# Performance work log

Measured on AMD Instinct MI355X. Metric: run time of the kernel, lower is better.

The kernel has to match this reference:

```python
import jax, jax.numpy as jnp
import numpy as np

TRIM_RATIO = 0.1
B, N, D_IN, D_H, N_OUT, D_OUT = 64, 1024, 512, 1024, 10, 1


def setup_inputs() -> dict:
    key = jax.random.key(0)
    ks = jax.random.split(key, 10)
    X = jax.random.normal(ks[0], (B, N, D_IN), dtype=jnp.float32)
    # ragged valid lengths in [N//2, N]; guarantees num_valid > 2*k for trim_ratio=0.1
    lengths = jax.random.randint(ks[1], (B,), N // 2, N + 1)
    mask = (jnp.arange(N)[None, :] < lengths[:, None]).astype(jnp.float32)
    s_in, s_h = 1.0 / np.sqrt(D_IN), 1.0 / np.sqrt(D_H)
    W1 = jax.random.uniform(ks[2], (D_IN, D_H), jnp.float32, -s_in, s_in)
    b1 = jax.random.uniform(ks[3], (D_H,), jnp.float32, -s_in, s_in)
    W2 = jax.random.uniform(ks[4], (D_H, D_H), jnp.float32, -s_h, s_h)
    b2 = jax.random.uniform(ks[5], (D_H,), jnp.float32, -s_h, s_h)
    W3 = jax.random.uniform(ks[6], (D_H, D_H), jnp.float32, -s_h, s_h)
    b3 = jax.random.uniform(ks[7], (D_H,), jnp.float32, -s_h, s_h)
    W4 = jax.random.uniform(ks[8], (D_H, N_OUT * D_OUT), jnp.float32, -s_h, s_h)
    b4 = jax.random.uniform(ks[9], (N_OUT * D_OUT,), jnp.float32, -s_h, s_h)
    return {"X": X, "mask": mask, "W1": W1, "b1": b1, "W2": W2, "b2": b2,
            "W3": W3, "b3": b3, "W4": W4, "b4": b4}


def reference(X, mask, W1, b1, W2, b2, W3, b3, W4, b4):
    # encode MLP: [B,N,D_IN] -> [B,N,D_H]
    encoded = jax.nn.relu(jnp.einsum('bni,ih->bnh', X, W1) + b1) @ W2 + b2
    masked = encoded * mask[..., None]
    num_valid = mask.sum(axis=-1).astype(jnp.int32)                 # [B]
    k = (num_valid.astype(jnp.float32) * TRIM_RATIO).astype(jnp.int32)  # floor, as int()
    # push invalid rows to +inf so valid elements occupy the first num_valid slots after sort
    padded = jnp.where(mask[..., None] > 0, masked, jnp.inf)
    sorted_v = jnp.sort(padded, axis=1)                             # per-column sort, [B,N,D_H]
    pos = jnp.arange(N)[None, :]
    keep = (pos >= k[:, None]) & (pos < (num_valid - k)[:, None])   # [B,N]
    summed = jnp.sum(jnp.where(keep[..., None], sorted_v, 0.0), axis=1)  # [B,D_H]
    denom = (num_valid - 2 * k).astype(jnp.float32)[:, None]
    aggregated = summed / denom                                     # trimmed mean
    # decode MLP
    out = jax.nn.relu(aggregated @ W3 + b3) @ W4 + b4               # [B, N_OUT*D_OUT]
    out = out.reshape(-1, N_OUT, D_OUT).squeeze(-1)                 # [B, N_OUT]
    return out
```

## Files before the change

kernel.cpp:

```cpp
#include <hip/hip_runtime.h>


typedef _Float16 half8  __attribute__((ext_vector_type(8)));
typedef _Float16 half4v __attribute__((ext_vector_type(4)));
typedef float    floatx4 __attribute__((ext_vector_type(4)));

#define GLD_LDS(g, l)                                                                     \
  __builtin_amdgcn_global_load_lds((const __attribute__((address_space(1))) void*)(g),    \
                                   (__attribute__((address_space(3))) void*)(l), 16, 0, 0)

__global__ void prep_nv(const float* __restrict__ mask, int* __restrict__ nv_arr,
                        int* __restrict__ k_arr) {
  int b = blockIdx.x, lane = threadIdx.x;
  const float4* mp = (const float4*)(mask + (b << 10));
  float s = 0.f;
#pragma unroll
  for (int i = 0; i < 4; ++i) {
    float4 v = mp[lane + i * 64];
    s += v.x + v.y + v.z + v.w;
  }
#pragma unroll
  for (int off = 32; off > 0; off >>= 1) s += __shfl_xor(s, off, 64);
  if (lane == 0) {
    int nv = (int)(s + 0.5f);
    int kk = (int)((float)nv * 0.1f);
    nv_arr[b] = nv;
    k_arr[b] = kk;
  }
}

__device__ __forceinline__ void transpose_body(const float* __restrict__ W,
                                               _Float16* __restrict__ WT, int R, int C,
                                               int r0, int c0, _Float16 (*tile)[65]) {
  for (int i = threadIdx.x; i < 4096; i += 256) {
    int r = i >> 6, c = i & 63;
    tile[r][c] = (_Float16)W[(size_t)(r0 + r) * C + c0 + c];
  }
  __syncthreads();
  for (int i = threadIdx.x; i < 4096; i += 256) {
    int c = i >> 6, r = i & 63;
    WT[(size_t)(c0 + c) * R + r0 + r] = tile[r][c];
  }
}

__global__ __launch_bounds__(256) void preprocess(
    const float* __restrict__ X, _Float16* __restrict__ X16,
    const float* __restrict__ W1, _Float16* __restrict__ W1T,
    const float* __restrict__ W2, _Float16* __restrict__ W2T,
    const int* __restrict__ nv_arr) {
  __shared__ _Float16 tile[64][65];
  int bid = blockIdx.x;
  if (bid < 16384) {
    int n0 = (bid << 2) & 1023;
    int batch = bid >> 8;
    int nv = nv_arr[batch];
    if (n0 >= ((nv + 255) & ~255)) return;
    int i = (bid * 256 + threadIdx.x) * 8;
    float4 a = *(const float4*)(X + i);
    float4 c = *(const float4*)(X + i + 4);
    half8 h;
    h[0] = (_Float16)a.x; h[1] = (_Float16)a.y; h[2] = (_Float16)a.z; h[3] = (_Float16)a.w;
    h[4] = (_Float16)c.x; h[5] = (_Float16)c.y; h[6] = (_Float16)c.z; h[7] = (_Float16)c.w;
    *(half8*)(X16 + i) = h;
  } else if (bid < 16384 + 128) {
    int id = bid - 16384;
    transpose_body(W1, W1T, 512, 1024, (id & 7) * 64, (id >> 3) * 64, tile);
  } else {
    int id = bid - 16512;
    transpose_body(W2, W2T, 1024, 1024, (id & 15) * 64, (id >> 4) * 64, tile);
  }
}

template <int KDIM, int MODE>
__global__ __launch_bounds__(512, 2) void gemm_kernel(
    const _Float16* __restrict__ Aop, const _Float16* __restrict__ Bop,
    const float* __restrict__ bias, const int* __restrict__ nv_arr,
    _Float16* __restrict__ outp) {
  constexpr int NT = KDIM / 64;
  __shared__ __align__(16) _Float16 lds[2][2][256 * 64];

  int bid = blockIdx.x;
  int fat = ((((bid >> 5) << 3) | (bid & 7))) << 8;
  int thin = ((bid >> 3) & 3) << 8;
  int i0, j0;
  if (MODE == 1) {
    i0 = thin; j0 = fat;
    if ((j0 & 1023) >= nv_arr[j0 >> 10]) return;
  } else {
    i0 = fat; j0 = thin;
    if ((i0 & 1023) >= nv_arr[i0 >> 10]) return;
  }
  const int t = threadIdx.x, lane = t & 63;
  const int wv = t >> 6, wm = wv & 1, wn = wv >> 1;
  const int lr = lane & 15, q = lane >> 4;
  const int swz = (q ^ (lr & 7)) * 8;

  const int gch = (t & 7) ^ ((t >> 3) & 7);
  const _Float16* gA = Aop + (size_t)(i0 + (t >> 3)) * KDIM + gch * 8;
  const _Float16* gB = Bop + (size_t)(j0 + (t >> 3)) * KDIM + gch * 8;

#define STG(OP, BUF, KT, R)                                                   \
  GLD_LDS(((OP) ? gB : gA) + (size_t)(R) * 64 * KDIM + (size_t)(KT) * 64,     \
          &lds[BUF][OP][((R) * 512 + (t & ~63)) * 8])

  floatx4 acc[8][4] = {};
  half8 af[4][2];
  half8 bf[2][2][2];

#define LD_A(BUF, IH)                                                         \
  _Pragma("unroll") for (int f = 0; f < 4; ++f)                               \
  _Pragma("unroll") for (int kk = 0; kk < 2; ++kk)                            \
      af[f][kk] = *(const half8*)&lds[BUF][0]                                 \
          [(((wm << 7) + ((IH) << 6) + (f << 4) + lr) << 6) + (swz ^ (kk << 5))];

#define LD_B(BUF, JH)                                                         \
  _Pragma("unroll") for (int g = 0; g < 2; ++g)                               \
  _Pragma("unroll") for (int kk = 0; kk < 2; ++kk)                            \
      bf[JH][g][kk] = *(const half8*)&lds[BUF][1]                             \
          [(((wn << 6) + ((JH) << 5) + (g << 4) + lr) << 6) + (swz ^ (kk << 5))];

#define MFMA_QUAD(IH, JH)                                                     \
  _Pragma("unroll") for (int f = 0; f < 4; ++f)                               \
  _Pragma("unroll") for (int g = 0; g < 2; ++g)                               \
  _Pragma("unroll") for (int kk = 0; kk < 2; ++kk)                            \
      acc[((IH) << 2) + f][((JH) << 1) + g] =                                 \
          __builtin_amdgcn_mfma_f32_16x16x32_f16(                             \
              af[f][kk], bf[JH][g][kk], acc[((IH) << 2) + f][((JH) << 1) + g], 0, 0, 0);

#define PHASE_TAIL(IH, JH)                                                    \
  __builtin_amdgcn_s_barrier();                                               \
  asm volatile("s_waitcnt lgkmcnt(0)" ::: "memory");                          \
  __builtin_amdgcn_sched_barrier(0);                                          \
  __builtin_amdgcn_s_setprio(1);                                              \
  MFMA_QUAD(IH, JH);                                                          \
  __builtin_amdgcn_s_setprio(0);                                              \
  __builtin_amdgcn_s_barrier();

#define BODY(KT, CUR, NXT, DO_A, DO_B, VMC)                                   \
  {                                                                           \
    LD_A(CUR, 0); LD_B(CUR, 0);                                               \
    if (DO_A) { STG(0, NXT, (KT) + 1, 0); STG(0, NXT, (KT) + 1, 1); }         \
    PHASE_TAIL(0, 0);                                                         \
    LD_B(CUR, 1);                                                             \
    if (DO_A) { STG(0, NXT, (KT) + 1, 2); STG(0, NXT, (KT) + 1, 3); }         \
    PHASE_TAIL(0, 1);                                                         \
    LD_A(CUR, 1);                                                             \
    if (DO_B) { STG(1, CUR, (KT) + 2, 0); STG(1, CUR, (KT) + 2, 1); }         \
    PHASE_TAIL(1, 0);                                                         \
    if (DO_B) { STG(1, CUR, (KT) + 2, 2); STG(1, CUR, (KT) + 2, 3); }         \
    asm volatile("s_waitcnt " VMC ::: "memory");                              \
    __builtin_amdgcn_sched_barrier(0);                                        \
    __builtin_amdgcn_s_setprio(1);                                            \
    MFMA_QUAD(1, 1);                                                          \
    __builtin_amdgcn_s_setprio(0);                                            \
    __builtin_amdgcn_s_barrier();                                             \
  }

  STG(0, 0, 0, 0); STG(0, 0, 0, 1); STG(0, 0, 0, 2); STG(0, 0, 0, 3);
  STG(1, 0, 0, 0); STG(1, 0, 0, 1); STG(1, 0, 0, 2); STG(1, 0, 0, 3);
  STG(1, 1, 1, 0); STG(1, 1, 1, 1); STG(1, 1, 1, 2); STG(1, 1, 1, 3);
  asm volatile("s_waitcnt vmcnt(4)" ::: "memory");
  __builtin_amdgcn_s_barrier();

  for (int kt = 0; kt < NT - 3; kt += 2) {
    BODY(kt, 0, 1, 1, 1, "vmcnt(4)");
    BODY(kt + 1, 1, 0, 1, 1, "vmcnt(4)");
  }
  BODY(NT - 2, 0, 1, 1, 0, "vmcnt(0)");
  BODY(NT - 1, 1, 0, 0, 0, "vmcnt(0)");

  if (MODE == 1) {
#pragma unroll
    for (int mi = 0; mi < 8; ++mi) {
      int ih = i0 + (wm << 7) + (mi << 4) + (q << 2);
      floatx4 bb = *(const floatx4*)&bias[ih];
#pragma unroll
      for (int nj = 0; nj < 4; ++nj) {
        int j = j0 + (wn << 6) + (nj << 4) + lr;
        floatx4 v = acc[mi][nj];
        half4v hv;
#pragma unroll
        for (int r = 0; r < 4; ++r) hv[r] = (_Float16)fmaxf(v[r] + bb[r], 0.f);
        *(half4v*)&outp[(size_t)j * 1024 + ih] = hv;
      }
    }
  } else {
#pragma unroll
    for (int nj = 0; nj < 4; ++nj) {
      int j = j0 + (wn << 6) + (nj << 4) + lr;
      float bj = bias[j];
#pragma unroll
      for (int mi = 0; mi < 8; ++mi) {
        int im = i0 + (wm << 7) + (mi << 4) + (q << 2);
        int bb = im >> 10, n = im & 1023;
        floatx4 v = acc[mi][nj];
        half4v hv;
#pragma unroll
        for (int r = 0; r < 4; ++r) hv[r] = (_Float16)(v[r] + bj);
        *(half4v*)&outp[((size_t)bb << 20) + ((size_t)j << 10) + (size_t)n] = hv;
      }
    }
  }
}

#define NB 1024
__global__ __launch_bounds__(256) void trim_kernel(const _Float16* __restrict__ encT,
                                                   const int* __restrict__ nv_arr,
                                                   const int* __restrict__ k_arr,
                                                   float* __restrict__ agg) {
  __shared__ unsigned int cnt[4 * NB];
  int t = threadIdx.x, lane = t & 63, w = t >> 6;
  int blk = blockIdx.x;
  int batch = blk >> 8;
  int h = ((blk & 255) << 2) + w;
  unsigned int* cw = cnt + w * NB;
  uint4* cp = (uint4*)cw;
  {
    uint4 z = {0u, 0u, 0u, 0u};
#pragma unroll
    for (int i = 0; i < 4; ++i) cp[lane * 4 + (i ^ ((lane >> 1) & 3))] = z;
  }

  int nv = nv_arr[batch], kk = k_arr[batch];
  const _Float16* col = encT + ((size_t)batch << 20) + ((size_t)h << 10);
  const uint4* p = (const uint4*)col + lane * 2;
  uint4 u0 = p[0], u1 = p[1];
  unsigned vals[8] = {u0.x, u0.y, u0.z, u0.w, u1.x, u1.y, u1.z, u1.w};
  int nvalid = nv - lane * 16;

  float vv[16];
  int bn[16];
#pragma unroll
  for (int d = 0; d < 8; ++d) {
    unsigned u = vals[d];
#pragma unroll
    for (int sub = 0; sub < 2; ++sub) {
      int idx = d * 2 + sub;
      unsigned short bits = (unsigned short)(sub ? (u >> 16) : (u & 0xffffu));
      _Float16 hvv;
      __builtin_memcpy(&hvv, &bits, 2);
      float v = (float)hvv;
      if (idx < nvalid) {
        v = fminf(fmaxf(v, -8.0f), 7.999f);
        int bin = (int)((v + 8.0f) * 64.0f);
        bin = min(NB - 1, bin);
        vv[idx] = v;
        bn[idx] = bin;
        int Lb = bin >> 4, jc = (bin >> 2) & 3;
        int phys = ((Lb << 2) + (jc ^ ((Lb >> 1) & 3))) * 4 + (bin & 3);
        atomicAdd(&cw[phys], 1u);
      } else {
        vv[idx] = 0.f;
        bn[idx] = -1;
      }
    }
  }

  int c[16];
  {
    uint4 rb[4];
#pragma unroll
    for (int i = 0; i < 4; ++i) rb[i] = cp[lane * 4 + (i ^ ((lane >> 1) & 3))];
#pragma unroll
    for (int i = 0; i < 4; ++i) {
      c[4 * i] = (int)rb[i].x; c[4 * i + 1] = (int)rb[i].y;
      c[4 * i + 2] = (int)rb[i].z; c[4 * i + 3] = (int)rb[i].w;
    }
  }
  int ct = 0;
#pragma unroll
  for (int i = 0; i < 16; ++i) ct += c[i];
  int ci = ct;
#pragma unroll
  for (int off = 1; off < 64; off <<= 1) {
    int cu = __shfl_up(ci, off, 64);
    if (lane >= off) ci += cu;
  }
  int cex = ci - ct;
  int r1 = kk, r2 = nv - kk;
  int p1 = -1, p2 = -1;
  {
    int run = cex;
#pragma unroll
    for (int i = 0; i < 16; ++i) {
      int cc = c[i];
      if (run < r1 && r1 <= run + cc) p1 = ((lane * 16 + i) << 12) | run;
      if (run < r2 && r2 <= run + cc) p2 = ((lane * 16 + i) << 12) | run;
      run += cc;
    }
  }
#pragma unroll
  for (int off = 32; off > 0; off >>= 1) {
    p1 = max(p1, __shfl_xor(p1, off, 64));
    p2 = max(p2, __shfl_xor(p2, off, 64));
  }
  int b1 = p1 >> 12, cex1 = p1 & 4095;
  int b2 = p2 >> 12, cex2 = p2 & 4095;
  float s1 = 0.f, s2 = 0.f, tm = 0.f;
  int c1 = 0, c2 = 0;
#pragma unroll
  for (int i = 0; i < 16; ++i) {
    int b = bn[i];
    float v = vv[i];
    if (b == b1) { s1 += v; c1++; }
    if (b == b2) { s2 += v; c2++; }
    if (b > b1 && b < b2) tm += v;
  }
#pragma unroll
  for (int off = 32; off > 0; off >>= 1) {
    s1 += __shfl_xor(s1, off, 64);
    s2 += __shfl_xor(s2, off, 64);
    tm += __shfl_xor(tm, off, 64);
    c1 += __shfl_xor(c1, off, 64);
    c2 += __shfl_xor(c2, off, 64);
  }
  float mid;
  if (b1 == b2) {
    mid = (float)(r2 - r1) * (s1 / (float)c1);
  } else {
    mid = (float)(cex1 + c1 - r1) * (s1 / (float)c1) + tm +
          (float)(r2 - cex2) * (s2 / (float)c2);
  }
  if (lane == 0) {
    agg[(batch << 10) + h] = mid / (float)(nv - 2 * kk);
  }
}

__global__ __launch_bounds__(256) void decode1(const float* __restrict__ agg,
                                               const float* __restrict__ W3,
                                               const float* __restrict__ b3,
                                               float* __restrict__ A3) {
  __shared__ float al[1024];
  __shared__ float red[256];
  int b = blockIdx.x, hb = blockIdx.y, t = threadIdx.x;
  for (int i = t; i < 1024; i += 256) al[i] = agg[(b << 10) + i];
  __syncthreads();
  int hl = t & 63, ks = t >> 6;
  int h = hb * 64 + hl;
  const float* wp = W3 + (size_t)(ks * 256) * 1024 + h;
  const float* ap = al + ks * 256;
  float acc = 0.f;
#pragma unroll 8
  for (int k = 0; k < 256; ++k) acc = fmaf(ap[k], wp[(size_t)k * 1024], acc);
  red[t] = acc;
  __syncthreads();
  if (t < 64) {
    float s = red[t] + red[t + 64] + red[t + 128] + red[t + 192] + b3[hb * 64 + t];
    A3[(b << 10) + hb * 64 + t] = fmaxf(s, 0.f);
  }
}

__global__ void decode2(const float* __restrict__ A3, const float* __restrict__ W4,
                        const float* __restrict__ b4, float* __restrict__ outp) {
  __shared__ float red[4][10];
  int b = blockIdx.x, t = threadIdx.x, lane = t & 63, w = t >> 6;
  float part[10];
#pragma unroll
  for (int o = 0; o < 10; ++o) part[o] = 0.f;
#pragma unroll
  for (int jj = 0; jj < 4; ++jj) {
    int h2 = jj * 256 + t;
    float a = A3[(b << 10) + h2];
#pragma unroll
    for (int o = 0; o < 10; ++o) part[o] = fmaf(a, W4[h2 * 10 + o], part[o]);
  }
#pragma unroll
  for (int o = 0; o < 10; ++o)
#pragma unroll
    for (int off = 32; off > 0; off >>= 1) part[o] += __shfl_xor(part[o], off, 64);
  if (lane == 0)
#pragma unroll
    for (int o = 0; o < 10; ++o) red[w][o] = part[o];
  __syncthreads();
  if (t < 10) outp[b * 10 + t] = b4[t] + red[0][t] + red[1][t] + red[2][t] + red[3][t];
}

extern "C" void kernel_launch(void* const* d_in, const int* in_sizes, int n_in,
                              void* d_out, int out_size, void* d_ws, size_t ws_size,
                              hipStream_t stream) {
  const float* X = (const float*)d_in[0];
  const float* mask = (const float*)d_in[1];
  const float* W1 = (const float*)d_in[2];
  const float* b1 = (const float*)d_in[3];
  const float* W2 = (const float*)d_in[4];
  const float* b2 = (const float*)d_in[5];
  const float* W3 = (const float*)d_in[6];
  const float* b3 = (const float*)d_in[7];
  const float* W4 = (const float*)d_in[8];
  const float* b4 = (const float*)d_in[9];
  float* outp = (float*)d_out;
  char* ws = (char*)d_ws;

  _Float16* X16 = (_Float16*)(ws);
  _Float16* H1 = (_Float16*)(ws + 67108864ull);
  _Float16* encT = (_Float16*)(ws + 201326592ull);
  _Float16* W1T = (_Float16*)(ws + 335544320ull);
  _Float16* W2T = (_Float16*)(ws + 336592896ull);
  float* agg = (float*)(ws + 338690048ull);
  float* A3 = (float*)(ws + 338952192ull);
  int* nv_arr = (int*)(ws + 339214336ull);
  int* k_arr = (int*)(ws + 339214592ull);

  prep_nv<<<64, 64, 0, stream>>>(mask, nv_arr, k_arr);
  preprocess<<<16768, 256, 0, stream>>>(X, X16, W1, W1T, W2, W2T, nv_arr);
  gemm_kernel<512, 1><<<1024, 512, 0, stream>>>(W1T, X16, b1, nv_arr, H1);
  gemm_kernel<1024, 2><<<1024, 512, 0, stream>>>(H1, W2T, b2, nv_arr, encT);
  trim_kernel<<<16384, 256, 0, stream>>>(encT, nv_arr, k_arr, agg);
  decode1<<<dim3(64, 16), 256, 0, stream>>>(agg, W3, b3, A3);
  decode2<<<64, 256, 0, stream>>>(A3, W4, b4, outp);
}
```

Baseline: 535.2 us.

## Restructure GEMM main loop into software-pipelined tiles with fewer barriers

Replaces the four-phase BODY loop, which had barriers around every MFMA quad, with a TILE schedule. Each tile issues LDS fragment loads for the next quad, or the next tile, while the current MFMAs run. Both A and B are now double-buffered two tiles ahead, and there are two barriers per tile instead of roughly seven. The aim is to cut barrier stalls and overlap LDS reads and global-to-LDS copies with matrix math. The cost is extra fragment registers (af_hi, bfB), which may raise VGPR pressure and lower occupancy, and the reuse of the current buffer for prefetch needs correct synchronisation.

```diff
diff --git a/kernel.cpp b/kernel.cpp
--- a/kernel.cpp
+++ b/kernel.cpp
@@ -104,70 +104,77 @@
           &lds[BUF][OP][((R) * 512 + (t & ~63)) * 8])
 
   floatx4 acc[8][4] = {};
-  half8 af[4][2];
-  half8 bf[2][2][2];
-
-#define LD_A(BUF, IH)                                                         \
+  half8 af_lo[4][2], af_hi[4][2];
+  half8 bfA[2][2][2], bfB[2][2][2];
+
+#define LD_A(BUF, IH, DST)                                                    \
   _Pragma("unroll") for (int f = 0; f < 4; ++f)                               \
   _Pragma("unroll") for (int kk = 0; kk < 2; ++kk)                            \
-      af[f][kk] = *(const half8*)&lds[BUF][0]                                 \
+      DST[f][kk] = *(const half8*)&lds[BUF][0]                                \
           [(((wm << 7) + ((IH) << 6) + (f << 4) + lr) << 6) + (swz ^ (kk << 5))];
 
-#define LD_B(BUF, JH)                                                         \
+#define LD_B_HALF(BUF, SET, JH)                                               \
   _Pragma("unroll") for (int g = 0; g < 2; ++g)                               \
   _Pragma("unroll") for (int kk = 0; kk < 2; ++kk)                            \
-      bf[JH][g][kk] = *(const half8*)&lds[BUF][1]                             \
+      SET[JH][g][kk] = *(const half8*)&lds[BUF][1]                            \
           [(((wn << 6) + ((JH) << 5) + (g << 4) + lr) << 6) + (swz ^ (kk << 5))];
 
-#define MFMA_QUAD(IH, JH)                                                     \
+#define MFMA_QUAD(IH, JH, AF, SET)                                            \
+  __builtin_amdgcn_s_setprio(1);                                              \
   _Pragma("unroll") for (int f = 0; f < 4; ++f)                               \
   _Pragma("unroll") for (int g = 0; g < 2; ++g)                               \
   _Pragma("unroll") for (int kk = 0; kk < 2; ++kk)                            \
       acc[((IH) << 2) + f][((JH) << 1) + g] =                                 \
           __builtin_amdgcn_mfma_f32_16x16x32_f16(                             \
-              af[f][kk], bf[JH][g][kk], acc[((IH) << 2) + f][((JH) << 1) + g], 0, 0, 0);
-
-#define PHASE_TAIL(IH, JH)                                                    \
-  __builtin_amdgcn_s_barrier();                                               \
-  asm volatile("s_waitcnt lgkmcnt(0)" ::: "memory");                          \
-  __builtin_amdgcn_sched_barrier(0);                                          \
-  __builtin_amdgcn_s_setprio(1);                                              \
-  MFMA_QUAD(IH, JH);                                                          \
-  __builtin_amdgcn_s_setprio(0);                                              \
-  __builtin_amdgcn_s_barrier();
-
-#define BODY(KT, CUR, NXT, DO_A, DO_B, VMC)                                   \
+              AF[f][kk], SET[JH][g][kk], acc[((IH) << 2) + f][((JH) << 1) + g], 0, 0, 0); \
+  __builtin_amdgcn_s_setprio(0);
+
+#define TILE(KT, CUR, NXT, BFC, BFN, DO_STG, DO_NEXT)                         \
   {                                                                           \
-    LD_A(CUR, 0); LD_B(CUR, 0);                                               \
-    if (DO_A) { STG(0, NXT, (KT) + 1, 0); STG(0, NXT, (KT) + 1, 1); }         \
-    PHASE_TAIL(0, 0);                                                         \
-    LD_B(CUR, 1);                                                             \
-    if (DO_A) { STG(0, NXT, (KT) + 1, 2); STG(0, NXT, (KT) + 1, 3); }         \
-    PHASE_TAIL(0, 1);                                                         \
-    LD_A(CUR, 1);                                                             \
-    if (DO_B) { STG(1, CUR, (KT) + 2, 0); STG(1, CUR, (KT) + 2, 1); }         \
-    PHASE_TAIL(1, 0);                                                         \
-    if (DO_B) { STG(1, CUR, (KT) + 2, 2); STG(1, CUR, (KT) + 2, 3); }         \
-    asm volatile("s_waitcnt " VMC ::: "memory");                              \
+                                                                      \
+    LD_B_HALF(CUR, BFC, 1);                                                   \
+    MFMA_QUAD(0, 0, af_lo, BFC);                                              \
+                                                                      \
+    LD_A(CUR, 1, af_hi);                                                      \
+    MFMA_QUAD(0, 1, af_lo, BFC);                                              \
+    asm volatile("s_waitcnt lgkmcnt(0)" ::: "memory");                        \
     __builtin_amdgcn_sched_barrier(0);                                        \
-    __builtin_amdgcn_s_setprio(1);                                            \
-    MFMA_QUAD(1, 1);                                                          \
-    __builtin_amdgcn_s_setprio(0);                                            \
-    __builtin_amdgcn_s_barrier();                                             \
+    __builtin_amdgcn_s_barrier();            \
+    __builtin_amdgcn_sched_barrier(0);                                        \
+                                                                      \
+    if (DO_STG) { STG(0, CUR, (KT) + 2, 0); STG(0, CUR, (KT) + 2, 1);         \
+                  STG(1, CUR, (KT) + 2, 0); STG(1, CUR, (KT) + 2, 1); }       \
+    MFMA_QUAD(1, 0, af_hi, BFC);                                              \
+    if (DO_NEXT) {                                                            \
+      if (DO_STG) { asm volatile("s_waitcnt vmcnt(4)" ::: "memory"); }        \
+      else        { asm volatile("s_waitcnt vmcnt(0)" ::: "memory"); }        \
+      __builtin_amdgcn_sched_barrier(0);                                      \
+      __builtin_amdgcn_s_barrier();                 \
+      __builtin_amdgcn_sched_barrier(0);                                      \
+    }                                                                         \
+                                                                      \
+    if (DO_STG) { STG(0, CUR, (KT) + 2, 2); STG(0, CUR, (KT) + 2, 3);         \
+                  STG(1, CUR, (KT) + 2, 2); STG(1, CUR, (KT) + 2, 3); }       \
+    if (DO_NEXT) { LD_A(NXT, 0, af_lo); LD_B_HALF(NXT, BFN, 0); }             \
+    MFMA_QUAD(1, 1, af_hi, BFC);                                              \
   }
 
   STG(0, 0, 0, 0); STG(0, 0, 0, 1); STG(0, 0, 0, 2); STG(0, 0, 0, 3);
   STG(1, 0, 0, 0); STG(1, 0, 0, 1); STG(1, 0, 0, 2); STG(1, 0, 0, 3);
+  STG(0, 1, 1, 0); STG(0, 1, 1, 1); STG(0, 1, 1, 2); STG(0, 1, 1, 3);
   STG(1, 1, 1, 0); STG(1, 1, 1, 1); STG(1, 1, 1, 2); STG(1, 1, 1, 3);
-  asm volatile("s_waitcnt vmcnt(4)" ::: "memory");
+  asm volatile("s_waitcnt vmcnt(8)" ::: "memory");
   __builtin_amdgcn_s_barrier();
-
-  for (int kt = 0; kt < NT - 3; kt += 2) {
-    BODY(kt, 0, 1, 1, 1, "vmcnt(4)");
-    BODY(kt + 1, 1, 0, 1, 1, "vmcnt(4)");
-  }
-  BODY(NT - 2, 0, 1, 1, 0, "vmcnt(0)");
-  BODY(NT - 1, 1, 0, 0, 0, "vmcnt(0)");
+  __builtin_amdgcn_sched_barrier(0);
+  LD_A(0, 0, af_lo);
+  LD_B_HALF(0, bfA, 0);
+
+  for (int kt = 0; kt < NT - 2; kt += 2) {
+    TILE(kt, 0, 1, bfA, bfB, 1, 1);
+    TILE(kt + 1, 1, 0, bfB, bfA, 1, 1);
+  }
+  TILE(NT - 2, 0, 1, bfA, bfB, 0, 1);
+  TILE(NT - 1, 1, 0, bfB, bfA, 0, 0);
 
   if (MODE == 1) {
 #pragma unroll
```

New measurement: 715.9 us. +33.8%, slower.
